# Performance work log

Measured on AMD Instinct MI355X. Metric: run time of the kernel, lower is better.

Reference implementation:

```python
import jax, jax.numpy as jnp
import numpy as np

FACTOR = 2  # upsample factor per spatial dim


def setup_inputs() -> dict:
    key = jax.random.key(0)
    k1, k2, k3 = jax.random.split(key, 3)
    B, C_in, C_out, H, W_ = 8, 128, 128, 64, 64
    x = jax.random.normal(k1, (B, C_in, H, W_), dtype=jnp.float32)
    # conv3x3 params (OIHW), fan-in scaled init like torch Conv2d default scale
    fan_in = C_in * 3 * 3
    W = jax.random.normal(k2, (C_out, C_in, 3, 3), dtype=jnp.float32) / np.sqrt(fan_in)
    b = jax.random.normal(k3, (C_out,), dtype=jnp.float32) * 0.01
    return {"x": x, "W": W, "b": b}


def reference(x, W, b):
    h = jnp.repeat(jnp.repeat(x, FACTOR, axis=2), FACTOR, axis=3)  # [B,C,2H,2W]
    # conv3x3: stride 1, padding 1
    out = jax.lax.conv_general_dilated(
        h, W,
        window_strides=(1, 1),
        padding=((1, 1), (1, 1)),
        dimension_numbers=("NCHW", "OIHW", "NCHW"),
    )
    return out + b[None, :, None, None]
```

## Files before the change

kernel.cpp:

```cpp
#include <hip/hip_runtime.h>
#include <stdint.h>

typedef short bf16x8 __attribute__((ext_vector_type(8)));
typedef float f32x4 __attribute__((ext_vector_type(4)));

#define NCI 128
#define NCO 128
#define HIN 64
#define HP  66
#define NB  8

__device__ __forceinline__ unsigned short f32_to_bf16(float f) {
    union { float f; uint32_t u; } v; v.f = f;
    return (unsigned short)((v.u + 0x7FFFu + ((v.u >> 16) & 1u)) >> 16);
}

__device__ __forceinline__ float weff_sum(const float* wp, int py, int px, int ty, int tx) {
    float s = 0.f;
    #pragma unroll
    for (int ky = 0; ky < 3; ++ky) {
        bool iy = (py == 0) ? (ty == 0 ? (ky == 0) : (ky >= 1))
                            : (ty == 0 ? (ky <= 1) : (ky == 2));
        if (!iy) continue;
        #pragma unroll
        for (int kx = 0; kx < 3; ++kx) {
            bool ix = (px == 0) ? (tx == 0 ? (kx == 0) : (kx >= 1))
                                : (tx == 0 ? (kx <= 1) : (kx == 2));
            if (ix) s += wp[ky * 3 + kx];
        }
    }
    return s;
}

__global__ __launch_bounds__(256) void prep_kernel(
        const float* __restrict__ W, const float* __restrict__ x,
        unsigned short* __restrict__ Aw5, unsigned short* __restrict__ xq) {
    if (blockIdx.x < 1024) {
        int idx = blockIdx.x * 256 + threadIdx.x;
        int e   = idx & 7;
        int rl  = (idx >> 3) & 15;
        int pl  = (idx >> 7) & 3;
        int f   = (idx >> 9) & 3;
        int wm  = (idx >> 11) & 1;
        int kt  = (idx >> 12) & 15;
        int par = idx >> 16;
        int co = wm * 64 + f * 16 + rl;
        int k  = kt * 32 + pl * 8 + e;
        int tap = k >> 7, ci = k & 127;
        Aw5[idx] = f32_to_bf16(weff_sum(W + (co * NCI + ci) * 9,
                                        par >> 1, par & 1, tap >> 1, tap & 1));
    } else {
        const int bb = blockIdx.x - 1024;
        const int b = bb / HP, hp = bb % HP;
        const int t = threadIdx.x;
        if (hp == 0 || hp == HP - 1) {
            bf16x8 z = (bf16x8){0, 0, 0, 0, 0, 0, 0, 0};
            for (int i = t; i < 4 * HP * 4; i += 256) {
                int g = i / (HP * 4), rem = i % (HP * 4);
                unsigned short* dst = xq +
                    ((((size_t)(b * 4 + g) * HP + hp) * HP) << 5) + rem * 8;
                *(bf16x8*)dst = z;
            }
            return;
        }
        const int h = hp - 1;
        if (t < 32) {
            bf16x8 z = (bf16x8){0, 0, 0, 0, 0, 0, 0, 0};
            int g = t >> 3, wpc = ((t >> 2) & 1) * (HP - 1), q = t & 3;
            unsigned short* dst = xq +
                ((((size_t)(b * 4 + g) * HP + hp) * HP + wpc) << 5) + q * 8;
            *(bf16x8*)dst = z;
        }
        const int w = t & 63, g = t >> 6;
        const float* src = x + ((size_t)(b * NCI + g * 32) * (HIN * HIN)) + h * HIN + w;
        unsigned short* dst = xq +
            ((((size_t)(b * 4 + g) * HP + hp) * HP + (w + 1)) << 5);
        #pragma unroll
        for (int q = 0; q < 4; ++q) {
            bf16x8 v;
            #pragma unroll
            for (int j = 0; j < 8; ++j)
                v[j] = (short)f32_to_bf16(src[(size_t)(q * 8 + j) * (HIN * HIN)]);
            *(bf16x8*)(dst + q * 8) = v;
        }
    }
}

__global__ __launch_bounds__(256, 4) void upconv12_kernel(
        const unsigned short* __restrict__ xq, const unsigned short* __restrict__ Aw5,
        const float* __restrict__ bv, float* __restrict__ out) {
    const int d = blockIdx.x;
    const int dsw = (d & 7) * 128 + (d >> 3);
    const int py = dsw & 1;
    const int t = dsw >> 1;
    const int bi = t >> 6;
    const int oy0 = t & 63;
    const int tid = threadIdx.x, lane = tid & 63, wv = tid >> 6;
    const int pxw = wv & 1, wm = wv >> 1;
    const int rl = lane & 15, pl = lane >> 4;
    const int par = py * 2 + pxw;

    const unsigned short* Ab = Aw5 + ((par * 16 * 2 + wm) << 11) + lane * 8;
    const char* xqb = (const char*)xq + (((size_t)bi * 4 * HP * HP) << 6);
    const int blane = rl * 64 + pl * 16;

    f32x4 acc[4][4];
    #pragma unroll
    for (int i = 0; i < 4; ++i)
        #pragma unroll
        for (int j = 0; j < 4; ++j)
            acc[i][j] = (f32x4){0.f, 0.f, 0.f, 0.f};

    bf16x8 A0[4], B0[4], B1[4];

    auto loadA = [&](int kt) {
        const unsigned short* p = Ab + (kt << 12);
        #pragma unroll
        for (int f = 0; f < 4; ++f)
            A0[f] = *(const bf16x8*)(p + f * 512);
    };
    auto loadB = [&](bf16x8* Bd, int kt) {
        const int row = oy0 + py + (kt >> 3);
        const int g = kt & 3;
        const int cb = pxw + ((kt >> 2) & 1);
        const char* base = xqb + (((g * HP + row) * HP + cb) << 6) + blane;
        #pragma unroll
        for (int fn = 0; fn < 4; ++fn)
            Bd[fn] = *(const bf16x8*)(base + fn * 1024);
    };

    #define MFMA_STEP(BB)                                                     \
        __builtin_amdgcn_s_setprio(1);                                        \
        _Pragma("unroll")                                                     \
        for (int fn = 0; fn < 4; ++fn) {                                      \
            _Pragma("unroll")                                                 \
            for (int fm = 0; fm < 4; ++fm)                                    \
                acc[fm][fn] = __builtin_amdgcn_mfma_f32_16x16x32_bf16(        \
                    A0[fm], BB[fn], acc[fm][fn], 0, 0, 0);                    \
        }                                                                     \
        __builtin_amdgcn_s_setprio(0);

    loadB(B0, 0);
    for (int kp = 0; kp < 8; ++kp) {
        int kt = kp * 2;
        loadA(kt);
        loadB(B1, kt + 1);
        asm volatile("s_waitcnt vmcnt(4)" ::: "memory");
        MFMA_STEP(B0)
        kt = kp * 2 + 1;
        loadA(kt);
        if (kp < 7) {
            loadB(B0, kt + 1);
            asm volatile("s_waitcnt vmcnt(4)" ::: "memory");
        } else {
            asm volatile("s_waitcnt vmcnt(0)" ::: "memory");
        }
        MFMA_STEP(B1)
    }
    #undef MFMA_STEP

    const int yy = 2 * oy0 + py;
    float* ob = out + (((size_t)bi * NCO + wm * 64 + pl * 4) << 14)
                    + yy * 128 + 2 * rl + pxw;
    #pragma unroll
    for (int fm = 0; fm < 4; ++fm) {
        #pragma unroll
        for (int j = 0; j < 4; ++j) {
            const float bb = bv[wm * 64 + fm * 16 + pl * 4 + j];
            float* o2 = ob + ((fm * 16 + j) << 14);
            #pragma unroll
            for (int fn = 0; fn < 4; ++fn)
                o2[fn * 32] = acc[fm][fn][j] + bb;
        }
    }
}

__global__ void weff_flat_kernel(const float* __restrict__ W,
                                 unsigned short* __restrict__ Aw) {
    int idx = blockIdx.x * 256 + threadIdx.x;
    int par = idx >> 16;
    int co  = (idx >> 9) & 127;
    int k   = idx & 511;
    int tap = k >> 7, ci = k & 127;
    Aw[idx] = f32_to_bf16(weff_sum(W + (co * NCI + ci) * 9,
                                   par >> 1, par & 1, tap >> 1, tap & 1));
}

__global__ __launch_bounds__(256) void upconv_fb_kernel(
        const float* __restrict__ x, const unsigned short* __restrict__ Aw,
        const float* __restrict__ bv, float* __restrict__ out) {
    __shared__ __align__(16) unsigned short A_lds[128 * 32];
    __shared__ __align__(16) unsigned short B_lds[128 * 32];
    const int par = blockIdx.y, py = par >> 1, px = par & 1;
    const int s0 = blockIdx.x * 128;
    const int bimg = s0 >> 12;
    const int oy0 = (s0 >> 6) & 63;
    const int tid = threadIdx.x;
    const int lane = tid & 63, wave = tid >> 6;
    const int wm = wave >> 1, wn = wave & 1;
    const float* xb = x + bimg * (NCI * HIN * HIN);
    f32x4 acc[4][4];
    #pragma unroll
    for (int i = 0; i < 4; ++i)
        #pragma unroll
        for (int j = 0; j < 4; ++j)
            acc[i][j] = (f32x4){0.f, 0.f, 0.f, 0.f};
    for (int kt = 0; kt < 16; ++kt) {
        const int tap = kt >> 2, ci0 = (kt & 3) * 32;
        const int ty = tap >> 1, tx = tap & 1;
        #pragma unroll
        for (int i = 0; i < 2; ++i) {
            int c = i * 256 + tid;
            *(bf16x8*)(&A_lds[c * 8]) = *(const bf16x8*)(Aw +
                ((par * 128 + (c >> 2)) * 512 + kt * 32 + (c & 3) * 8));
        }
        #pragma unroll
        for (int i = 0; i < 2; ++i) {
            int tsk = i * 256 + tid;
            int n = tsk & 127, kg = tsk >> 7;
            int r = n >> 6, ox = n & 63;
            int row = oy0 + r - 1 + py + ty;
            int col = ox - 1 + px + tx;
            bool ok = (row >= 0) & (row < HIN) & (col >= 0) & (col < HIN);
            const float* xp = xb + (((ci0 + kg * 8) * HIN + row) * HIN + col);
            bf16x8 v;
            #pragma unroll
            for (int q = 0; q < 8; ++q) {
                float f = ok ? xp[q * (HIN * HIN)] : 0.f;
                v[q] = (short)f32_to_bf16(f);
            }
            *(bf16x8*)(&B_lds[n * 32 + kg * 8]) = v;
        }
        __syncthreads();
        const int seg = (lane >> 4) * 8, rl2 = lane & 15;
        bf16x8 af[4], bfr[4];
        #pragma unroll
        for (int f = 0; f < 4; ++f)
            af[f] = *(const bf16x8*)(&A_lds[(wm * 64 + f * 16 + rl2) * 32 + seg]);
        #pragma unroll
        for (int f = 0; f < 4; ++f)
            bfr[f] = *(const bf16x8*)(&B_lds[(wn * 64 + f * 16 + rl2) * 32 + seg]);
        #pragma unroll
        for (int fm = 0; fm < 4; ++fm)
            #pragma unroll
            for (int fn = 0; fn < 4; ++fn)
                acc[fm][fn] = __builtin_amdgcn_mfma_f32_16x16x32_bf16(
                    af[fm], bfr[fn], acc[fm][fn], 0, 0, 0);
        __syncthreads();
    }
    #pragma unroll
    for (int fm = 0; fm < 4; ++fm) {
        const int co_b = wm * 64 + fm * 16 + (lane >> 4) * 4;
        float bias4[4];
        #pragma unroll
        for (int j = 0; j < 4; ++j) bias4[j] = bv[co_b + j];
        #pragma unroll
        for (int fn = 0; fn < 4; ++fn) {
            int n = wn * 64 + fn * 16 + (lane & 15);
            int s = s0 + n;
            int ox = s & 63, oy = (s >> 6) & 63, bi2 = s >> 12;
            int yy = 2 * oy + py, xx = 2 * ox + px;
            float* op = out + ((size_t)bi2 * 128 * 128 * 128) + (size_t)yy * 128 + xx;
            #pragma unroll
            for (int j = 0; j < 4; ++j)
                op[(size_t)(co_b + j) * (128 * 128)] = acc[fm][fn][j] + bias4[j];
        }
    }
}

extern "C" void kernel_launch(void* const* d_in, const int* in_sizes, int n_in,
                              void* d_out, int out_size, void* d_ws, size_t ws_size,
                              hipStream_t stream) {
    const float* x  = (const float*)d_in[0];
    const float* W  = (const float*)d_in[1];
    const float* bv = (const float*)d_in[2];
    float* out = (float*)d_out;
    unsigned short* Aw = (unsigned short*)d_ws;
    const size_t aw_bytes = (size_t)4 * 16 * 2 * 2048 * sizeof(unsigned short);
    const size_t xq_bytes = (size_t)NB * 4 * HP * HP * 32 * sizeof(unsigned short);

    if (ws_size >= aw_bytes + xq_bytes) {
        unsigned short* xq = (unsigned short*)((char*)d_ws + aw_bytes);
        prep_kernel<<<1024 + NB * HP, 256, 0, stream>>>(W, x, Aw, xq);
        upconv12_kernel<<<1024, 256, 0, stream>>>(xq, Aw, bv, out);
    } else {
        weff_flat_kernel<<<1024, 256, 0, stream>>>(W, Aw);
        upconv_fb_kernel<<<dim3(256, 4), 256, 0, stream>>>(x, Aw, bv, out);
    }
}
```

Measured before the change: 47.16 us.

## Split output channels across two blocks, double-buffer A, use nontemporal stores

Each block now computes 64 output channels instead of 128: the grid doubles to 2048 blocks and each wave holds a 32-channel by 64-pixel tile. The weight layout in the prep kernel changes to match. The K loop is fully unrolled with double-buffered A and B registers and loads issued two steps ahead, replacing the manual vmcnt waits. Output writes use nontemporal stores. The aim is more parallelism and fewer registers per wave, at the cost of each B (input) tile being loaded by twice as many blocks.

Result: slower. 65.28 us (+38.4%).

```diff
diff --git a/kernel.cpp b/kernel.cpp
--- a/kernel.cpp
+++ b/kernel.cpp
@@ -34,20 +34,20 @@
 
 __global__ __launch_bounds__(256) void prep_kernel(
         const float* __restrict__ W, const float* __restrict__ x,
-        unsigned short* __restrict__ Aw5, unsigned short* __restrict__ xq) {
+        unsigned short* __restrict__ Aw6, unsigned short* __restrict__ xq) {
     if (blockIdx.x < 1024) {
         int idx = blockIdx.x * 256 + threadIdx.x;
         int e   = idx & 7;
         int rl  = (idx >> 3) & 15;
         int pl  = (idx >> 7) & 3;
-        int f   = (idx >> 9) & 3;
-        int wm  = (idx >> 11) & 1;
+        int f   = (idx >> 9) & 1;
+        int cob = (idx >> 10) & 3;
         int kt  = (idx >> 12) & 15;
         int par = idx >> 16;
-        int co = wm * 64 + f * 16 + rl;
+        int co = cob * 32 + f * 16 + rl;
         int k  = kt * 32 + pl * 8 + e;
         int tap = k >> 7, ci = k & 127;
-        Aw5[idx] = f32_to_bf16(weff_sum(W + (co * NCI + ci) * 9,
+        Aw6[idx] = f32_to_bf16(weff_sum(W + (co * NCI + ci) * 9,
                                         par >> 1, par & 1, tap >> 1, tap & 1));
     } else {
         const int bb = blockIdx.x - 1024;
@@ -86,38 +86,39 @@
     }
 }
 
-__global__ __launch_bounds__(256, 4) void upconv12_kernel(
-        const unsigned short* __restrict__ xq, const unsigned short* __restrict__ Aw5,
+__global__ __launch_bounds__(256, 4) void upconv13_kernel(
+        const unsigned short* __restrict__ xq, const unsigned short* __restrict__ Aw6,
         const float* __restrict__ bv, float* __restrict__ out) {
     const int d = blockIdx.x;
-    const int dsw = (d & 7) * 128 + (d >> 3);
+    const int cob2 = d & 1;
+    const int dd = d >> 1;
+    const int dsw = (dd & 7) * 128 + (dd >> 3);
     const int py = dsw & 1;
     const int t = dsw >> 1;
-    const int bi = t >> 6;
-    const int oy0 = t & 63;
+    const int bi = t >> 6, oy0 = t & 63;
     const int tid = threadIdx.x, lane = tid & 63, wv = tid >> 6;
-    const int pxw = wv & 1, wm = wv >> 1;
+    const int pxw = wv & 1, cobL = wv >> 1;
+    const int cob = cob2 * 2 + cobL;
     const int rl = lane & 15, pl = lane >> 4;
     const int par = py * 2 + pxw;
 
-    const unsigned short* Ab = Aw5 + ((par * 16 * 2 + wm) << 11) + lane * 8;
+    const unsigned short* Ab = Aw6 + (((par * 16 * 4) + cob) << 10) + lane * 8;
     const char* xqb = (const char*)xq + (((size_t)bi * 4 * HP * HP) << 6);
     const int blane = rl * 64 + pl * 16;
 
-    f32x4 acc[4][4];
-    #pragma unroll
-    for (int i = 0; i < 4; ++i)
+    f32x4 acc[2][4];
+    #pragma unroll
+    for (int i = 0; i < 2; ++i)
         #pragma unroll
         for (int j = 0; j < 4; ++j)
             acc[i][j] = (f32x4){0.f, 0.f, 0.f, 0.f};
 
-    bf16x8 A0[4], B0[4], B1[4];
-
-    auto loadA = [&](int kt) {
+    bf16x8 A0[2], A1[2], B0[4], B1[4];
+
+    auto loadA = [&](bf16x8* Ad, int kt) {
         const unsigned short* p = Ab + (kt << 12);
-        #pragma unroll
-        for (int f = 0; f < 4; ++f)
-            A0[f] = *(const bf16x8*)(p + f * 512);
+        Ad[0] = *(const bf16x8*)p;
+        Ad[1] = *(const bf16x8*)(p + 512);
     };
     auto loadB = [&](bf16x8* Bd, int kt) {
         const int row = oy0 + py + (kt >> 3);
@@ -129,48 +130,41 @@
             Bd[fn] = *(const bf16x8*)(base + fn * 1024);
     };
 
-    #define MFMA_STEP(BB)                                                     \
-        __builtin_amdgcn_s_setprio(1);                                        \
-        _Pragma("unroll")                                                     \
-        for (int fn = 0; fn < 4; ++fn) {                                      \
-            _Pragma("unroll")                                                 \
-            for (int fm = 0; fm < 4; ++fm)                                    \
-                acc[fm][fn] = __builtin_amdgcn_mfma_f32_16x16x32_bf16(        \
-                    A0[fm], BB[fn], acc[fm][fn], 0, 0, 0);                    \
-        }                                                                     \
+    loadB(B0, 0);
+    loadA(A0, 0);
+    loadB(B1, 1);
+    loadA(A1, 1);
+
+    #pragma unroll
+    for (int kp = 0; kp < 16; ++kp) {
+        bf16x8* Ac = (kp & 1) ? A1 : A0;
+        bf16x8* Bc = (kp & 1) ? B1 : B0;
+        __builtin_amdgcn_s_setprio(1);
+        #pragma unroll
+        for (int fn = 0; fn < 4; ++fn)
+            #pragma unroll
+            for (int fm = 0; fm < 2; ++fm)
+                acc[fm][fn] = __builtin_amdgcn_mfma_f32_16x16x32_bf16(
+                    Ac[fm], Bc[fn], acc[fm][fn], 0, 0, 0);
         __builtin_amdgcn_s_setprio(0);
-
-    loadB(B0, 0);
-    for (int kp = 0; kp < 8; ++kp) {
-        int kt = kp * 2;
-        loadA(kt);
-        loadB(B1, kt + 1);
-        asm volatile("s_waitcnt vmcnt(4)" ::: "memory");
-        MFMA_STEP(B0)
-        kt = kp * 2 + 1;
-        loadA(kt);
-        if (kp < 7) {
-            loadB(B0, kt + 1);
-            asm volatile("s_waitcnt vmcnt(4)" ::: "memory");
-        } else {
-            asm volatile("s_waitcnt vmcnt(0)" ::: "memory");
-        }
-        MFMA_STEP(B1)
-    }
-    #undef MFMA_STEP
+        if (kp + 2 < 16) {
+            loadB(Bc, kp + 2);
+            loadA(Ac, kp + 2);
+        }
+    }
 
     const int yy = 2 * oy0 + py;
-    float* ob = out + (((size_t)bi * NCO + wm * 64 + pl * 4) << 14)
+    float* ob = out + (((size_t)(bi * NCO + cob * 32 + pl * 4)) << 14)
                     + yy * 128 + 2 * rl + pxw;
     #pragma unroll
-    for (int fm = 0; fm < 4; ++fm) {
+    for (int fm = 0; fm < 2; ++fm) {
         #pragma unroll
         for (int j = 0; j < 4; ++j) {
-            const float bb = bv[wm * 64 + fm * 16 + pl * 4 + j];
-            float* o2 = ob + ((fm * 16 + j) << 14);
+            const float bb = bv[cob * 32 + fm * 16 + pl * 4 + j];
+            float* o2 = ob + (((size_t)(fm * 16 + j)) << 14);
             #pragma unroll
             for (int fn = 0; fn < 4; ++fn)
-                o2[fn * 32] = acc[fm][fn][j] + bb;
+                __builtin_nontemporal_store(acc[fm][fn][j] + bb, o2 + fn * 32);
         }
     }
 }
@@ -276,13 +270,13 @@
     const float* bv = (const float*)d_in[2];
     float* out = (float*)d_out;
     unsigned short* Aw = (unsigned short*)d_ws;
-    const size_t aw_bytes = (size_t)4 * 16 * 2 * 2048 * sizeof(unsigned short);
+    const size_t aw_bytes = (size_t)4 * 16 * 4 * 1024 * sizeof(unsigned short);
     const size_t xq_bytes = (size_t)NB * 4 * HP * HP * 32 * sizeof(unsigned short);
 
     if (ws_size >= aw_bytes + xq_bytes) {
         unsigned short* xq = (unsigned short*)((char*)d_ws + aw_bytes);
         prep_kernel<<<1024 + NB * HP, 256, 0, stream>>>(W, x, Aw, xq);
-        upconv12_kernel<<<1024, 256, 0, stream>>>(xq, Aw, bv, out);
+        upconv13_kernel<<<2048, 256, 0, stream>>>(xq, Aw, bv, out);
     } else {
         weff_flat_kernel<<<1024, 256, 0, stream>>>(W, Aw);
         upconv_fb_kernel<<<dim3(256, 4), 256, 0, stream>>>(x, Aw, bv, out);
```
